# Optimization experiments

Measured on AMD Instinct MI355X. Metric: run time of the kernel, lower is better.

Reference implementation:

```python
import jax, jax.numpy as jnp
import numpy as np
import math

B = 2000000
TWO_PI = 2.0 * math.pi

# ---- e3nn so3 generator construction (numpy, done once at import) ----

def _su2_generators(j):
    m = np.arange(-j, j)
    raising = np.diag(-np.sqrt(j * (j + 1) - m * (m + 1)), k=-1).astype(np.complex128)
    m = np.arange(-j + 1, j + 1)
    lowering = np.diag(np.sqrt(j * (j + 1) - m * (m - 1)), k=1).astype(np.complex128)
    m = np.arange(-j, j + 1)
    return np.stack([0.5 * (raising + lowering), np.diag(1j * m), -0.5j * (raising - lowering)])

def _change_basis_real_to_complex(l):
    q = np.zeros((2 * l + 1, 2 * l + 1), dtype=np.complex128)
    for m in range(-l, 0):
        q[l + m, l + abs(m)] = 1 / 2 ** 0.5
        q[l + m, l - abs(m)] = -1j / 2 ** 0.5
    q[l, l] = 1
    for m in range(1, l + 1):
        q[l + m, l + abs(m)] = (-1) ** m / 2 ** 0.5
        q[l + m, l - abs(m)] = 1j * (-1) ** m / 2 ** 0.5
    return (-1j) ** l * q

def _so3_generators(l):
    X = _su2_generators(l)
    Q = _change_basis_real_to_complex(l)
    return np.real(np.conj(Q.T) @ X @ Q)  # (3, 2l+1, 2l+1); X[0]=x-gen, X[1]=y-gen

def _eig_decomp(X):
    # X real antisymmetric with exact eigenvalues i*m; exp(a*X) = V diag(e^{a w}) V^-1
    w, V = np.linalg.eig(X.astype(np.complex128))
    w = 1j * np.round(w.imag)  # snap to exact i*m
    Vinv = np.linalg.inv(V)
    return (jnp.asarray(w, jnp.complex64), jnp.asarray(V, jnp.complex64), jnp.asarray(Vinv, jnp.complex64))

_GEN = {}
for _l in (4, 6):
    _X = _so3_generators(_l)
    _GEN[_l] = (_eig_decomp(_X[1]), _eig_decomp(_X[0]))  # (y-generator, x-generator)

# ---- rotations / angles (e3nn conventions) ----

def _quat_to_matrix(q):
    # e3nn: angle = 2*acos(clamp(w)), axis = normalize(q[1:]), Rodrigues
    angle = 2.0 * jnp.arccos(jnp.clip(q[..., 0], -1.0, 1.0))
    axis = q[..., 1:]
    axis = axis / jnp.maximum(jnp.linalg.norm(axis, axis=-1, keepdims=True), 1e-12)
    x, y, z = axis[..., 0], axis[..., 1], axis[..., 2]
    c, s = jnp.cos(angle), jnp.sin(angle)
    C = 1.0 - c
    return jnp.stack([
        jnp.stack([c + x * x * C, x * y * C - z * s, x * z * C + y * s], -1),
        jnp.stack([y * x * C + z * s, c + y * y * C, y * z * C - x * s], -1),
        jnp.stack([z * x * C - y * s, z * y * C + x * s, c + z * z * C], -1),
    ], -2)

def _matrix_y(a):
    c, s = jnp.cos(a), jnp.sin(a)
    o, z = jnp.ones_like(a), jnp.zeros_like(a)
    return jnp.stack([jnp.stack([c, z, s], -1), jnp.stack([z, o, z], -1), jnp.stack([-s, z, c], -1)], -2)

def _matrix_x(a):
    c, s = jnp.cos(a), jnp.sin(a)
    o, z = jnp.ones_like(a), jnp.zeros_like(a)
    return jnp.stack([jnp.stack([o, z, z], -1), jnp.stack([z, c, -s], -1), jnp.stack([z, s, c], -1)], -2)

def _xyz_to_angles(xyz):
    n = jnp.linalg.norm(xyz, axis=-1, keepdims=True)
    xyz = jnp.clip(xyz / jnp.maximum(n, 1e-12), -1.0, 1.0)
    beta = jnp.arccos(xyz[..., 1])
    alpha = jnp.arctan2(xyz[..., 0], xyz[..., 2])
    return alpha, beta

def _matrix_to_angles(R):
    x = R[..., :, 1]  # R @ [0,1,0]
    a, b = _xyz_to_angles(x)
    M = jnp.swapaxes(_matrix_y(a) @ _matrix_x(b), -1, -2) @ R
    c = jnp.arctan2(M[..., 0, 2], M[..., 0, 0])
    return a, b, c

# ---- Wigner-D applied to a fixed vector (fused matvec chain) ----

def _rot_apply(decomp, angle, v):
    # exp(angle*X) @ v via precomputed eigendecomposition; result is real
    w, V, Vinv = decomp
    u = jnp.einsum('mj,bj->bm', Vinv, v.astype(jnp.complex64))
    u = u * jnp.exp(angle[:, None].astype(jnp.complex64) * w)
    return jnp.real(jnp.einsum('im,bm->bi', V, u))

def _wigner_apply(l, alpha, beta, gamma, s):
    # D_l(alpha,beta,gamma) @ s = exp(a*Y) exp(b*X) exp(g*Y) @ s
    dy, dx = _GEN[l]
    v = jnp.broadcast_to(s, (alpha.shape[0], s.shape[0]))
    v = _rot_apply(dy, gamma % TWO_PI, v)
    v = _rot_apply(dx, beta % TWO_PI, v)
    v = _rot_apply(dy, alpha % TWO_PI, v)
    return v


def setup_inputs() -> dict:
    key = jax.random.key(0)
    k1, k2, k3 = jax.random.split(key, 3)
    quats = jax.random.normal(k1, (B, 4), dtype=jnp.float32)
    quats = quats / jnp.linalg.norm(quats, axis=-1, keepdims=True)  # unit quaternions
    s4 = jax.random.normal(k2, (9,), dtype=jnp.float32)
    s6 = jax.random.normal(k3, (13,), dtype=jnp.float32)
    return {"quats": quats, "s4": s4, "s6": s6}


def reference(quats, s4, s6):
    R = _quat_to_matrix(quats)
    alpha, beta, gamma = _matrix_to_angles(R)
    f4 = _wigner_apply(4, alpha, beta, gamma, s4)  # (B, 9)
    f6 = _wigner_apply(6, alpha, beta, gamma, s6)  # (B, 13)
    return (f4, f6)
```

## Files before the change

kernel.cpp:

```cpp
#include <hip/hip_runtime.h>
#include <math.h>

#define INV_SQRT2 0.70710678118654752440
#define PI_D 3.14159265358979323846

template <int N> struct MatF { float a[N * N]; };

constexpr double csqrt(double x) {
  if (x <= 0.0) return 0.0;
  double g = x > 1.0 ? x : 1.0;
  for (int i = 0; i < 40; ++i) g = 0.5 * (g + x / g);
  return g;
}

template <int L>
constexpr MatF<2 * L + 1> makeJ() {
  constexpr int n = 2 * L + 1;
  double Qr[n * n] = {}, Qi[n * n] = {};
  for (int r = 0; r < n; ++r) {
    int m = r - L;
    if (m < 0) {
      Qr[r * n + (L - m)] = INV_SQRT2;
      Qi[r * n + (L + m)] = -INV_SQRT2;
    } else if (m == 0) {
      Qr[r * n + L] = 1.0;
    } else {
      double sgn = (m & 1) ? -1.0 : 1.0;
      Qr[r * n + (L + m)] = sgn * INV_SQRT2;
      Qi[r * n + (L - m)] = sgn * INV_SQRT2;
    }
  }
  double c[n] = {};
  for (int i = 0; i + 1 < n; ++i) {
    double m = (double)(i - L);
    c[i] = 0.5 * csqrt((double)(L * (L + 1)) - m * (m + 1.0));
  }
  double Br[n * n] = {}, Bi[n * n] = {};
  for (int i = 0; i < n; ++i)
    for (int j = 0; j < n; ++j) {
      double br = 0, bi = 0;
      if (i + 1 < n) { br += c[i] * Qr[(i + 1) * n + j]; bi += c[i] * Qi[(i + 1) * n + j]; }
      if (i >= 1)    { br -= c[i - 1] * Qr[(i - 1) * n + j]; bi -= c[i - 1] * Qi[(i - 1) * n + j]; }
      Br[i * n + j] = br;
      Bi[i * n + j] = bi;
    }
  double A[n * n] = {};
  for (int i = 0; i < n; ++i)
    for (int j = 0; j < n; ++j) {
      double acc = 0;
      for (int k = 0; k < n; ++k)
        acc += Qr[k * n + i] * Br[k * n + j] + Qi[k * n + i] * Bi[k * n + j];
      if (j == 2 * L - i && i != L) acc += (double)(L - i);
      A[i * n + j] = acc * (PI_D * INV_SQRT2) * (1.0 / 64.0);
    }
  double T[n * n] = {}, U[n * n] = {};
  for (int i = 0; i < n; ++i) T[i * n + i] = 1.0;
  for (int k = 10; k >= 1; --k) {
    for (int i = 0; i < n; ++i)
      for (int j = 0; j < n; ++j) {
        double acc = 0;
        for (int q = 0; q < n; ++q) acc += A[i * n + q] * T[q * n + j];
        U[i * n + j] = acc;
      }
    double inv = 1.0 / (double)k;
    for (int i = 0; i < n; ++i)
      for (int j = 0; j < n; ++j)
        T[i * n + j] = ((i == j) ? 1.0 : 0.0) + U[i * n + j] * inv;
  }
  for (int s = 0; s < 6; ++s) {
    for (int i = 0; i < n; ++i)
      for (int j = 0; j < n; ++j) {
        double acc = 0;
        for (int q = 0; q < n; ++q) acc += T[i * n + q] * T[q * n + j];
        U[i * n + j] = acc;
      }
    for (int t = 0; t < n * n; ++t) T[t] = U[t];
  }
  MatF<n> R = {};
  for (int t = 0; t < n * n; ++t) {
    double v = T[t];
    if (v < 1e-9 && v > -1e-9) v = 0.0;
    R.a[t] = (float)v;
  }
  return R;
}

template <int L> struct JMat { static constexpr MatF<2 * L + 1> M = makeJ<L>(); };

template <int L, int I, int K>
__device__ __forceinline__ float matJ_dot(const float* v) {
  if constexpr (K < 0) {
    return 0.f;
  } else {
    float acc = matJ_dot<L, I, K - 1>(v);
    constexpr float w = JMat<L>::M.a[I * (2 * L + 1) + K];
    if constexpr (w != 0.0f) acc = fmaf(w, v[K], acc);
    return acc;
  }
}

template <int L, int I>
__device__ __forceinline__ void matJ_rows(const float* v, float* o) {
  if constexpr (I >= 0) {
    matJ_rows<L, I - 1>(v, o);
    o[I] = matJ_dot<L, I, 2 * L>(v);
  }
}

template <int L>
__device__ __forceinline__ void matJ(const float* v, float* o) {
  matJ_rows<L, 2 * L>(v, o);
}

template <int L>
__device__ __forceinline__ void rotY(float c1, float s1, const float* v, float* o) {
  o[L] = v[L];
  float ck = c1, sk = s1;
#pragma unroll
  for (int k = 1; k <= L; k++) {
    o[L - k] = ck * v[L - k] + sk * v[L + k];
    o[L + k] = -sk * v[L - k] + ck * v[L + k];
    float cn = ck * c1 - sk * s1;
    sk = sk * c1 + ck * s1;
    ck = cn;
  }
}

template <int L>
__device__ __forceinline__ void wigner_apply(const float* __restrict__ svec,
                                             float ca, float sa, float cb, float sb,
                                             float cg, float sg, float* f) {
  constexpr int n = 2 * L + 1;
  float t[n], u[n], sv[n];
#pragma unroll
  for (int k = 0; k < n; k++) sv[k] = svec[k];
  rotY<L>(cg, sg, sv, t);
  matJ<L>(t, u);
  rotY<L>(cb, sb, u, t);
  matJ<L>(t, u);
  rotY<L>(ca, sa, u, f);
}

__global__ __launch_bounds__(256) void wigner_main(
    const float4* __restrict__ quats,
    const float* __restrict__ s4,
    const float* __restrict__ s6,
    float* __restrict__ out,
    int B) {
  __shared__ float lds[2304 + 3328];
  const int t = threadIdx.x;
  const int b = blockIdx.x;
  const int i = b * 256 + t;
  const int idx = (i < B) ? i : (B - 1);
  float4 q = quats[idx];

  float w = fminf(fmaxf(q.x, -1.f), 1.f);
  float c = 2.f * w * w - 1.f;
  float s = 2.f * w * sqrtf(fmaxf(1.f - w * w, 0.f));
  float an2 = q.y * q.y + q.z * q.z + q.w * q.w;
  float inv = (an2 > 1e-24f) ? rsqrtf(an2) : 1e12f;
  float ax = q.y * inv, ay = q.z * inv, az = q.w * inv;
  float C = 1.f - c;
  float R00 = c + ax * ax * C, R01 = ax * ay * C - az * s, R02 = ax * az * C + ay * s;
  float R20 = az * ax * C - ay * s, R21 = az * ay * C + ax * s, R22 = c + az * az * C;
  float R11 = c + ay * ay * C;

  float vx = R01, vy = R11, vz = R21;
  float n2 = vx * vx + vy * vy + vz * vz;
  float invn = (n2 > 1e-24f) ? rsqrtf(n2) : 1e12f;
  vx = fminf(fmaxf(vx * invn, -1.f), 1.f);
  vy = fminf(fmaxf(vy * invn, -1.f), 1.f);
  vz = fminf(fmaxf(vz * invn, -1.f), 1.f);
  float cb = vy;
  float sb = sqrtf(fmaxf(1.f - cb * cb, 0.f));
  float h2 = vx * vx + vz * vz;
  float ca, sa;
  if (h2 > 1e-30f) { float rh = rsqrtf(h2); ca = vz * rh; sa = vx * rh; }
  else             { ca = 1.f; sa = 0.f; }
  float M00 = ca * R00 - sa * R20;
  float M02 = ca * R02 - sa * R22;
  float g2 = M00 * M00 + M02 * M02;
  float cg, sg;
  if (g2 > 1e-30f) { float rg = rsqrtf(g2); cg = M00 * rg; sg = M02 * rg; }
  else             { cg = 1.f; sg = 0.f; }

  wigner_apply<4>(s4, ca, sa, cb, sb, cg, sg, &lds[t * 9]);
  wigner_apply<6>(s6, ca, sa, cb, sb, cg, sg, &lds[2304 + t * 13]);
  __syncthreads();

  const bool full = (b + 1) * 256 <= B;
  if (full && (B & 3) == 0) {
    const float4* l4 = (const float4*)lds;
    float4* o4 = (float4*)(out + (size_t)b * 2304);
#pragma unroll
    for (int v = t; v < 576; v += 256) o4[v] = l4[v];
    const float4* l6 = (const float4*)(lds + 2304);
    float4* o6 = (float4*)(out + (size_t)B * 9 + (size_t)b * 3328);
#pragma unroll
    for (int v = t; v < 832; v += 256) o6[v] = l6[v];
  } else if (i < B) {
    float* o4 = out + (size_t)i * 9;
#pragma unroll
    for (int j = 0; j < 9; j++) o4[j] = lds[t * 9 + j];
    float* o6 = out + (size_t)B * 9 + (size_t)i * 13;
#pragma unroll
    for (int j = 0; j < 13; j++) o6[j] = lds[2304 + t * 13 + j];
  }
}

extern "C" void kernel_launch(void* const* d_in, const int* in_sizes, int n_in,
                              void* d_out, int out_size, void* d_ws, size_t ws_size,
                              hipStream_t stream) {
  const float4* quats = (const float4*)d_in[0];
  const float* s4 = (const float*)d_in[1];
  const float* s6 = (const float*)d_in[2];
  float* out = (float*)d_out;
  int B = in_sizes[0] / 4;
  int blocks = (B + 255) / 256;
  hipLaunchKernelGGL(wigner_main, dim3(blocks), dim3(256), 0, stream,
                     quats, s4, s6, out, B);
}
```

Baseline: 195.0 us.

## Share precomputed trig tables and overlap l=6 stores with l=4 compute

Precomputes the multiple-angle cos/sin tables once per rotation angle and shares them between the l=4 and l=6 paths instead of recomputing recurrences inside each rotY. Splits LDS into separate buffers so the l=6 result is written out before the l=4 work is computed, letting global stores overlap with arithmetic. Uses nontemporal vector stores and adds a min-blocks launch bound of 4, which may constrain registers. The extra barrier and more live registers for the trig tables could reduce occupancy.

```diff
diff --git a/kernel.cpp b/kernel.cpp
--- a/kernel.cpp
+++ b/kernel.cpp
@@ -3,6 +3,8 @@
 
 #define INV_SQRT2 0.70710678118654752440
 #define PI_D 3.14159265358979323846
+
+typedef float vfloat4 __attribute__((ext_vector_type(4)));
 
 template <int N> struct MatF { float a[N * N]; };
 
@@ -112,42 +114,51 @@
   matJ_rows<L, 2 * L>(v, o);
 }
 
-template <int L>
-__device__ __forceinline__ void rotY(float c1, float s1, const float* v, float* o) {
+struct Trig { float c[7]; float s[7]; };
+
+__device__ __forceinline__ Trig mk_trig(float c1, float s1) {
+  Trig t;
+  t.c[0] = 1.f; t.s[0] = 0.f;
+  t.c[1] = c1;  t.s[1] = s1;
+#pragma unroll
+  for (int k = 2; k <= 6; ++k) {
+    t.c[k] = t.c[k - 1] * c1 - t.s[k - 1] * s1;
+    t.s[k] = t.s[k - 1] * c1 + t.c[k - 1] * s1;
+  }
+  return t;
+}
+
+template <int L>
+__device__ __forceinline__ void rotY(const Trig& tg, const float* v, float* o) {
   o[L] = v[L];
-  float ck = c1, sk = s1;
 #pragma unroll
   for (int k = 1; k <= L; k++) {
-    o[L - k] = ck * v[L - k] + sk * v[L + k];
-    o[L + k] = -sk * v[L - k] + ck * v[L + k];
-    float cn = ck * c1 - sk * s1;
-    sk = sk * c1 + ck * s1;
-    ck = cn;
+    o[L - k] =  tg.c[k] * v[L - k] + tg.s[k] * v[L + k];
+    o[L + k] = -tg.s[k] * v[L - k] + tg.c[k] * v[L + k];
   }
 }
 
 template <int L>
 __device__ __forceinline__ void wigner_apply(const float* __restrict__ svec,
-                                             float ca, float sa, float cb, float sb,
-                                             float cg, float sg, float* f) {
+                                             const Trig& ta, const Trig& tb,
+                                             const Trig& tg, float* f) {
   constexpr int n = 2 * L + 1;
-  float t[n], u[n], sv[n];
-#pragma unroll
-  for (int k = 0; k < n; k++) sv[k] = svec[k];
-  rotY<L>(cg, sg, sv, t);
+  float t[n], u[n];
+  rotY<L>(tg, svec, t);
   matJ<L>(t, u);
-  rotY<L>(cb, sb, u, t);
+  rotY<L>(tb, u, t);
   matJ<L>(t, u);
-  rotY<L>(ca, sa, u, f);
-}
-
-__global__ __launch_bounds__(256) void wigner_main(
+  rotY<L>(ta, u, f);
+}
+
+__global__ __launch_bounds__(256, 4) void wigner_main(
     const float4* __restrict__ quats,
     const float* __restrict__ s4,
     const float* __restrict__ s6,
     float* __restrict__ out,
     int B) {
-  __shared__ float lds[2304 + 3328];
+  __shared__ __align__(16) float lds6[256 * 13];
+  __shared__ __align__(16) float lds4[256 * 9];
   const int t = threadIdx.x;
   const int b = blockIdx.x;
   const int i = b * 256 + t;
@@ -184,27 +195,38 @@
   if (g2 > 1e-30f) { float rg = rsqrtf(g2); cg = M00 * rg; sg = M02 * rg; }
   else             { cg = 1.f; sg = 0.f; }
 
-  wigner_apply<4>(s4, ca, sa, cb, sb, cg, sg, &lds[t * 9]);
-  wigner_apply<6>(s6, ca, sa, cb, sb, cg, sg, &lds[2304 + t * 13]);
+  Trig TA = mk_trig(ca, sa);
+  Trig TB = mk_trig(cb, sb);
+  Trig TG = mk_trig(cg, sg);
+
+  const bool full4 = ((b + 1) * 256 <= B) && ((B & 3) == 0);
+
+  wigner_apply<6>(s6, TA, TB, TG, &lds6[t * 13]);
   __syncthreads();
-
-  const bool full = (b + 1) * 256 <= B;
-  if (full && (B & 3) == 0) {
-    const float4* l4 = (const float4*)lds;
-    float4* o4 = (float4*)(out + (size_t)b * 2304);
-#pragma unroll
-    for (int v = t; v < 576; v += 256) o4[v] = l4[v];
-    const float4* l6 = (const float4*)(lds + 2304);
-    float4* o6 = (float4*)(out + (size_t)B * 9 + (size_t)b * 3328);
-#pragma unroll
-    for (int v = t; v < 832; v += 256) o6[v] = l6[v];
+  if (full4) {
+    const vfloat4* l6 = (const vfloat4*)lds6;
+    vfloat4* o6 = (vfloat4*)(out + (size_t)B * 9 + (size_t)b * 3328);
+#pragma unroll
+    for (int v = t; v < 832; v += 256)
+      __builtin_nontemporal_store(l6[v], &o6[v]);
+  } else if (i < B) {
+    float* o6 = out + (size_t)B * 9 + (size_t)i * 13;
+#pragma unroll
+    for (int j = 0; j < 13; j++) o6[j] = lds6[t * 13 + j];
+  }
+
+  wigner_apply<4>(s4, TA, TB, TG, &lds4[t * 9]);
+  __syncthreads();
+  if (full4) {
+    const vfloat4* l4 = (const vfloat4*)lds4;
+    vfloat4* o4 = (vfloat4*)(out + (size_t)b * 2304);
+#pragma unroll
+    for (int v = t; v < 576; v += 256)
+      __builtin_nontemporal_store(l4[v], &o4[v]);
   } else if (i < B) {
     float* o4 = out + (size_t)i * 9;
 #pragma unroll
-    for (int j = 0; j < 9; j++) o4[j] = lds[t * 9 + j];
-    float* o6 = out + (size_t)B * 9 + (size_t)i * 13;
-#pragma unroll
-    for (int j = 0; j < 13; j++) o6[j] = lds[2304 + t * 13 + j];
+    for (int j = 0; j < 9; j++) o4[j] = lds4[t * 9 + j];
   }
 }
 
```

After: 198.8 us. Within noise of the previous version (+1.9%).
